# Kernel tuning notes

Hardware: AMD Instinct MI355X
Metric: run time of the kernel (lower is better)

Reference implementation:

```python
import jax, jax.numpy as jnp
import numpy as np

DIM = 512
CODEBOOK_SIZE = 2048
NUM_Q = 8
COMMIT_W = 0.25
B, T = 8, 2048


def setup_inputs() -> dict:
    key = jax.random.key(0)
    k1, k2 = jax.random.split(key)
    x = jax.random.normal(k1, (B, T, DIM), dtype=jnp.float32)
    lim = 1.0 / CODEBOOK_SIZE
    codebooks = jax.random.uniform(k2, (NUM_Q, CODEBOOK_SIZE, DIM), dtype=jnp.float32,
                                   minval=-lim, maxval=lim)
    return {"x": x, "codebooks": codebooks}


def reference(x, codebooks):
    """Residual VQ forward.
    x: (B, T, D); codebooks: (Q, K, D).
    Returns (quantized (B,T,D), indices (B,T,Q) int32, mean loss scalar).
    """
    sg = jax.lax.stop_gradient
    residual = x
    quantized = jnp.zeros_like(x)
    idx_list = []
    total_loss = jnp.zeros((), dtype=x.dtype)
    for i in range(NUM_Q):
        cb = codebooks[i]  # (K, D)
        # squared L2 distances: (B,T,K)
        d = (jnp.sum(residual * residual, axis=-1, keepdims=True)
             - 2.0 * jnp.einsum('btd,kd->btk', residual, cb)
             + jnp.sum(cb * cb, axis=-1))
        min_idx = jnp.argmin(d, axis=-1)  # (B,T)
        idx_list.append(min_idx)
        q_lvl = cb[min_idx]  # (B,T,D) gather
        quantized = quantized + q_lvl
        commit_loss = jnp.mean((sg(residual) - q_lvl) ** 2)
        codebook_loss = jnp.mean((residual - sg(q_lvl)) ** 2)
        total_loss = total_loss + commit_loss * COMMIT_W + codebook_loss
        residual = residual - sg(q_lvl)
    # straight-through estimator
    quantized = x + sg(quantized - x)
    indices = jnp.stack(idx_list, axis=-1)  # (B,T,Q)
    return quantized, indices, total_loss / NUM_Q
```

## Files before the change

kernel.cpp:

```cpp
#include <hip/hip_runtime.h>


constexpr int DIM   = 512;
constexpr int KCB   = 2048;
constexpr int NQ    = 8;
constexpr int NTOK  = 8 * 2048;
constexpr int QELEM = NTOK * DIM;
constexpr int NBLK2 = KCB / 256;
constexpr float WINDOW = 1e-3f;

using short8  = __attribute__((ext_vector_type(8))) short;
using float4v = __attribute__((ext_vector_type(4))) float;

__device__ __forceinline__ unsigned short f2bf(float f) {
    unsigned u = __float_as_uint(f);
    return (unsigned short)((u + 0x7FFFu + ((u >> 16) & 1u)) >> 16);
}

__device__ __forceinline__ void gl2lds16(const void* g, void* l) {
    __builtin_amdgcn_global_load_lds(
        (__attribute__((address_space(1))) void*)g,
        (__attribute__((address_space(3))) void*)l, 16, 0, 0);
}

struct Top4 { float s[4]; int i[4]; };
__device__ __forceinline__ void t4_init(Top4& t) {
#pragma unroll
    for (int j = 0; j < 4; ++j) { t.s[j] = 3.0e38f; t.i[j] = 0x7FFFFFFF; }
}
__device__ __forceinline__ void t4_ins(Top4& t, float s, int idx) {
    if (s < t.s[3]) {
        if (s < t.s[2]) { t.s[3] = t.s[2]; t.i[3] = t.i[2];
            if (s < t.s[1]) { t.s[2] = t.s[1]; t.i[2] = t.i[1];
                if (s < t.s[0]) { t.s[1] = t.s[0]; t.i[1] = t.i[0]; t.s[0] = s; t.i[0] = idx; }
                else            { t.s[1] = s; t.i[1] = idx; }
            } else { t.s[2] = s; t.i[2] = idx; }
        } else { t.s[3] = s; t.i[3] = idx; }
    }
}

__global__ __launch_bounds__(256) void k_initnorm(
        const float* __restrict__ x, const float* __restrict__ cbs,
        float4* __restrict__ R, ushort4* __restrict__ Rb, ushort4* __restrict__ Cbb,
        float* __restrict__ r2, float* __restrict__ c2)
{
#pragma clang fp contract(off)
    __shared__ float buf[4][DIM];
    __shared__ float accs[4][32];
    const int w = threadIdx.x >> 6, lane = threadIdx.x & 63;
    const bool isX = blockIdx.x < (NTOK / 4);
    const int row = (isX ? blockIdx.x : blockIdx.x - NTOK / 4) * 4 + w;

    const float* src = isX ? x : cbs;
    const float4* a4 = reinterpret_cast<const float4*>(src + (size_t)row * DIM);
    float4 v0 = a4[lane], v1 = a4[lane + 64];

    ushort4 b0 = make_ushort4(f2bf(v0.x), f2bf(v0.y), f2bf(v0.z), f2bf(v0.w));
    ushort4 b1 = make_ushort4(f2bf(v1.x), f2bf(v1.y), f2bf(v1.z), f2bf(v1.w));
    if (isX) {
        R [(size_t)row * 128 + lane]      = v0;
        R [(size_t)row * 128 + lane + 64] = v1;
        Rb[(size_t)row * 128 + lane]      = b0;
        Rb[(size_t)row * 128 + lane + 64] = b1;
    } else {
        Cbb[(size_t)row * 128 + lane]      = b0;
        Cbb[(size_t)row * 128 + lane + 64] = b1;
    }

    float4* b4 = reinterpret_cast<float4*>(buf[w]);
    b4[lane]      = v0;
    b4[lane + 64] = v1;
    __syncthreads();
    if (lane < 32) {
        int blk = lane >> 3, j = lane & 7;
        const float* p = buf[w] + blk * 128 + j;
        float x0 = p[0];
        float acc = x0 * x0;
#pragma unroll
        for (int m = 1; m < 16; ++m) { float xx = p[8 * m]; acc = acc + xx * xx; }
        accs[w][lane] = acc;
    }
    __syncthreads();
    if (lane == 0) {
        float B[4];
#pragma unroll
        for (int blk = 0; blk < 4; ++blk) {
            const float* r = &accs[w][blk * 8];
            B[blk] = ((r[0] + r[1]) + (r[2] + r[3])) + ((r[4] + r[5]) + (r[6] + r[7]));
        }
        float out = (B[0] + B[1]) + (B[2] + B[3]);
        if (isX) r2[row] = out; else c2[row] = out;
    }
}

__global__ __launch_bounds__(512, 2) void k_gemm_topk(
        const unsigned short* __restrict__ Rb, const unsigned short* __restrict__ Cbb,
        const float* __restrict__ c2, float* __restrict__ candS, int* __restrict__ candI)
{
    __shared__ __align__(16) char smem[99328];
    unsigned short* As = (unsigned short*)smem;
    unsigned short* Bs = (unsigned short*)(smem + 49152);
    float*  scb = (float*)smem;
    float*  c2s = (float*)(smem + 98304);

    const int tid  = threadIdx.x;
    const int wid  = tid >> 6, lane = tid & 63;
    const int quad = lane >> 4, l16 = lane & 15;
    const int wr = wid >> 2, wc = wid & 3;

    const int L    = blockIdx.y * NBLK2 + blockIdx.x;
    const int slot = L >> 3;
    const int mb   = (L & 7) * 8 + (slot >> 3);
    const int nb2  = slot & 7;

    const int tok0 = mb * 256, n0 = nb2 * 256;

    if (tid < 256) c2s[tid] = c2[n0 + tid];

    float4v acc[8][4];
    float4v zero = {0.f, 0.f, 0.f, 0.f};
#pragma unroll
    for (int mi = 0; mi < 8; ++mi)
#pragma unroll
        for (int nj = 0; nj < 4; ++nj) acc[mi][nj] = zero;

    auto stage = [&](int b3, int kb) {
        unsigned short* Ad = As + b3 * 8192;
        unsigned short* Bd = Bs + b3 * 8192;
#pragma unroll
        for (int c = 0; c < 2; ++c) {
            int g = wid * 2 + c;
            gl2lds16(&Rb[(size_t)(tok0 + g * 16 + l16) * DIM + kb + quad * 8],
                     Ad + (size_t)(g * 64) * 8);
        }
#pragma unroll
        for (int c = 0; c < 2; ++c) {
            int g = wid * 2 + c;
            gl2lds16(&Cbb[(size_t)(n0 + g * 16 + l16) * DIM + kb + quad * 8],
                     Bd + (size_t)(g * 64) * 8);
        }
    };

    auto compute = [&](int b3) {
        const unsigned short* Ac = As + b3 * 8192;
        const unsigned short* Bc = Bs + b3 * 8192;
        short8 af[8], bf[4];
#pragma unroll
        for (int mi = 0; mi < 8; ++mi)
            af[mi] = *(const short8*)(Ac + ((size_t)(wr * 8 + mi) * 64 + lane) * 8);
#pragma unroll
        for (int nj = 0; nj < 4; ++nj)
            bf[nj] = *(const short8*)(Bc + ((size_t)(wc * 4 + nj) * 64 + lane) * 8);
        __builtin_amdgcn_s_setprio(1);
#pragma unroll
        for (int mi = 0; mi < 8; ++mi)
#pragma unroll
            for (int nj = 0; nj < 4; ++nj)
                acc[mi][nj] = __builtin_amdgcn_mfma_f32_16x16x32_bf16(
                    af[mi], bf[nj], acc[mi][nj], 0, 0, 0);
        __builtin_amdgcn_s_setprio(0);
    };

    stage(0, 0);
    stage(1, 32);
    for (int it = 0; it < 16; ++it) {
        if (it < 15) asm volatile("s_waitcnt vmcnt(4)" ::: "memory");
        else         asm volatile("s_waitcnt vmcnt(0)" ::: "memory");
        __builtin_amdgcn_s_barrier();
        __builtin_amdgcn_sched_barrier(0);
        if (it < 14) stage((it + 2) % 3, (it + 2) * 32);
        compute(it % 3);
    }

    const int row_ = tid >> 3, pp = tid & 7;
    float4 c2r[8];
#pragma unroll
    for (int j = 0; j < 8; ++j)
        c2r[j] = *(const float4*)(c2s + pp * 32 + 4 * j);

#pragma unroll
    for (int qr = 0; qr < 4; ++qr) {
        __syncthreads();
        if (wr == (qr >> 1)) {
            const int mi0 = (qr & 1) * 4;
#pragma unroll
            for (int mm = 0; mm < 4; ++mm)
#pragma unroll
                for (int nj = 0; nj < 4; ++nj) {
                    int r0 = mm * 16 + quad * 4;
                    int cc = wc * 64 + nj * 16 + l16;
#pragma unroll
                    for (int e = 0; e < 4; ++e)
                        scb[(r0 + e) * 260 + cc] = acc[mi0 + mm][nj][e];
                }
        }
        __syncthreads();
        Top4 t; t4_init(t);
#pragma unroll
        for (int j = 0; j < 8; ++j) {
            float4 sv = *(const float4*)(scb + row_ * 260 + pp * 32 + 4 * j);
            float4 cv = c2r[j];
            int c0 = n0 + pp * 32 + 4 * j;
            t4_ins(t, cv.x - 2.0f * sv.x, c0 + 0);
            t4_ins(t, cv.y - 2.0f * sv.y, c0 + 1);
            t4_ins(t, cv.z - 2.0f * sv.z, c0 + 2);
            t4_ins(t, cv.w - 2.0f * sv.w, c0 + 3);
        }
#pragma unroll
        for (int k = 1; k <= 2; k <<= 1) {
            float os[4]; int oi[4];
#pragma unroll
            for (int j = 0; j < 4; ++j) {
                os[j] = __shfl_xor(t.s[j], k, 64);
                oi[j] = __shfl_xor(t.i[j], k, 64);
            }
#pragma unroll
            for (int j = 0; j < 4; ++j) t4_ins(t, os[j], oi[j]);
        }
        if ((pp & 3) == 0) {
            int token = tok0 + qr * 64 + row_;
            int nb = nb2 * 2 + (pp >> 2);
            size_t base = (size_t)token * 64 + (size_t)nb * 4;
#pragma unroll
            for (int j = 0; j < 4; ++j) { candS[base + j] = t.s[j]; candI[base + j] = t.i[j]; }
        }
    }
}

__global__ __launch_bounds__(256) void k_selupd(
        const float* __restrict__ candS, const int* __restrict__ candI,
        float* __restrict__ R, const float* __restrict__ cbf,
        float* __restrict__ r2, const float* __restrict__ c2,
        float* __restrict__ idx_out, float* __restrict__ partial,
        ushort4* __restrict__ Rb, const float4* __restrict__ x, int level)
{
#pragma clang fp contract(off)
    __shared__ float buf[4][DIM];
    __shared__ float accs[4][32];
    __shared__ float shl[4];
    const int w = threadIdx.x >> 6, lane = threadIdx.x & 63;
    const int t = blockIdx.x * 4 + w;
    const bool last = (level == NQ - 1);

    float4* r4 = reinterpret_cast<float4*>(R + (size_t)t * DIM);
    float4* b4 = reinterpret_cast<float4*>(buf[w]);
    float4 rr[2];
    rr[0] = r4[lane];      rr[1] = r4[lane + 64];
    b4[lane] = rr[0];      b4[lane + 64] = rr[1];

    float sb = candS[(size_t)t * 64 + lane];
    int   ci = candI[(size_t)t * 64 + lane];
    float mn = sb;
#pragma unroll
    for (int off = 32; off; off >>= 1) mn = fminf(mn, __shfl_xor(mn, off, 64));
    unsigned long long mask = __ballot(sb <= mn + WINDOW);
    int ncand = __popcll(mask);
    int winner;
    if (ncand == 1) {
        winner = __shfl(ci, __ffsll(mask) - 1, 64);
    } else {
        int src = 0;
        if (lane < ncand) {
            unsigned long long mm = mask;
            for (int z = 0; z < lane; ++z) mm &= mm - 1;
            src = __ffsll(mm) - 1;
        }
        int cidx = __shfl(ci, src, 64);
        float s = 3.0e38f;
        int   si = 0x7FFFFFFF;
        if (lane < ncand) {
            const float4* cp4 = reinterpret_cast<const float4*>(cbf + (size_t)cidx * DIM);
            const float4* rp4 = reinterpret_cast<const float4*>(buf[w]);
            float d = 0.f;
#pragma unroll 4
            for (int j = 0; j < DIM / 4; ++j) {
                float4 cv = cp4[j];
                float4 rv = rp4[j];
                d = fmaf(rv.x, cv.x, d);
                d = fmaf(rv.y, cv.y, d);
                d = fmaf(rv.z, cv.z, d);
                d = fmaf(rv.w, cv.w, d);
            }
            float td = 2.0f * d;
            float a  = r2[t] - td;
            s  = a + c2[cidx];
            si = cidx;
        }
#pragma unroll
        for (int off = 32; off; off >>= 1) {
            float ov = __shfl_xor(s, off, 64);
            int   oi = __shfl_xor(si, off, 64);
            if (ov < s || (ov == s && oi < si)) { s = ov; si = oi; }
        }
        winner = si;
    }
    if (lane == 0) idx_out[(size_t)t * NQ + level] = (float)winner;

    const float4* c4 = reinterpret_cast<const float4*>(cbf + (size_t)winner * DIM);
    float ls = 0.f;
#pragma unroll
    for (int i = 0; i < 2; ++i) {
        int d = lane + 64 * i;
        float4 rv = rr[i], cv = c4[d];
        rv.x -= cv.x; rv.y -= cv.y; rv.z -= cv.z; rv.w -= cv.w;
        ls = ls + rv.x * rv.x; ls = ls + rv.y * rv.y;
        ls = ls + rv.z * rv.z; ls = ls + rv.w * rv.w;
        if (!last) {
            r4[d] = rv;
            b4[d] = rv;
            Rb[(size_t)t * 128 + d] = make_ushort4(f2bf(rv.x), f2bf(rv.y),
                                                   f2bf(rv.z), f2bf(rv.w));
        } else {
            float4 xv = x[(size_t)t * 128 + d];
            xv.x -= rv.x; xv.y -= rv.y; xv.z -= rv.z; xv.w -= rv.w;
            r4[d] = xv;
        }
    }

    if (!last) {
        __syncthreads();
        if (lane < 32) {
            int blk = lane >> 3, j = lane & 7;
            const float* p = buf[w] + blk * 128 + j;
            float x0 = p[0];
            float acc = x0 * x0;
#pragma unroll
            for (int m = 1; m < 16; ++m) { float xx = p[8 * m]; acc = acc + xx * xx; }
            accs[w][lane] = acc;
        }
        __syncthreads();
        if (lane == 0) {
            float B[4];
#pragma unroll
            for (int blk = 0; blk < 4; ++blk) {
                const float* r = &accs[w][blk * 8];
                B[blk] = ((r[0] + r[1]) + (r[2] + r[3])) + ((r[4] + r[5]) + (r[6] + r[7]));
            }
            r2[t] = (B[0] + B[1]) + (B[2] + B[3]);
        }
    }

#pragma unroll
    for (int off = 32; off; off >>= 1) ls += __shfl_down(ls, off, 64);
    if (lane == 0) shl[w] = ls;
    __syncthreads();
    if (threadIdx.x == 0) partial[blockIdx.x] = (shl[0] + shl[1]) + (shl[2] + shl[3]);
}

__global__ __launch_bounds__(256) void k_finalize_loss(const float* __restrict__ partial,
                                                       float* __restrict__ loss_out)
{
    double s = 0.0;
    for (int i = threadIdx.x; i < NQ * (NTOK / 4); i += 256) s += (double)partial[i];
#pragma unroll
    for (int off = 32; off; off >>= 1) s += __shfl_down(s, off, 64);
    __shared__ double sh[4];
    if ((threadIdx.x & 63) == 0) sh[threadIdx.x >> 6] = s;
    __syncthreads();
    if (threadIdx.x == 0) {
        double tot = (sh[0] + sh[1]) + (sh[2] + sh[3]);
        loss_out[0] = (float)(tot * 1.25 / ((double)NQ * (double)QELEM));
    }
}

extern "C" void kernel_launch(void* const* d_in, const int* in_sizes, int n_in,
                              void* d_out, int out_size, void* d_ws, size_t ws_size,
                              hipStream_t stream)
{
    const float* x   = (const float*)d_in[0];
    const float* cbs = (const float*)d_in[1];

    float* qout     = (float*)d_out;
    float* idx_out  = qout + QELEM;
    float* loss_out = idx_out + (size_t)NTOK * NQ;
    float* R        = qout;

    char* ws = (char*)d_ws;
    size_t off = 0;
    unsigned short* Rb   = (unsigned short*)(ws + off); off += (size_t)QELEM * 2;
    unsigned short* Cbb  = (unsigned short*)(ws + off); off += (size_t)QELEM * 2;
    float*          c2   = (float*)(ws + off);          off += (size_t)NQ * KCB * 4;
    float*          r2   = (float*)(ws + off);          off += (size_t)NTOK * 4;
    float*          part = (float*)(ws + off);          off += (size_t)NQ * (NTOK / 4) * 4;
    float*          candS= (float*)(ws + off);          off += (size_t)NTOK * 64 * 4;
    int*            candI= (int*)(ws + off);            off += (size_t)NTOK * 64 * 4;

    k_initnorm<<<NTOK / 4 + NQ * KCB / 4, 256, 0, stream>>>(
        x, cbs, (float4*)R, (ushort4*)Rb, (ushort4*)Cbb, r2, c2);

    for (int q = 0; q < NQ; ++q) {
        const float*          cbq  = cbs + (size_t)q * KCB * DIM;
        const unsigned short* cbbq = Cbb + (size_t)q * KCB * DIM;
        const float*          c2q  = c2 + (size_t)q * KCB;
        dim3 g(NBLK2, NTOK / 256);
        k_gemm_topk<<<g, 512, 0, stream>>>(Rb, cbbq, c2q, candS, candI);
        k_selupd<<<NTOK / 4, 256, 0, stream>>>(candS, candI, R, cbq, r2, c2q,
                                               idx_out, part + (size_t)q * (NTOK / 4),
                                               (ushort4*)Rb, (const float4*)x, q);
    }

    k_finalize_loss<<<1, 256, 0, stream>>>(part, loss_out);
}
```

Before: 992.6 us.

## Switch GEMM staging to double-buffered 64-wide K tiles with padded c2 layout

Replaces the triple-buffered K=32 staging pipeline, which used explicit vmcnt waits, with a double-buffered K=64 pipeline that loads two 32-wide halves per stage and synchronises with a plain __syncthreads. The aim is to halve the number of barrier iterations and do more MFMA work per sync. It also pads the shared c2 array by 4 floats per 32 entries to cut LDS bank conflicts on the float4 reads. The cost is LDS growing to about 132 KB per block, which likely allows only one block per CU instead of the two requested by launch_bounds. The plain __syncthreads may also drain outstanding loads and shrink the overlap between loads and compute.

```diff
diff --git a/kernel.cpp b/kernel.cpp
--- a/kernel.cpp
+++ b/kernel.cpp
@@ -97,11 +97,11 @@
         const unsigned short* __restrict__ Rb, const unsigned short* __restrict__ Cbb,
         const float* __restrict__ c2, float* __restrict__ candS, int* __restrict__ candI)
 {
-    __shared__ __align__(16) char smem[99328];
+    __shared__ __align__(16) char smem[132224];
     unsigned short* As = (unsigned short*)smem;
-    unsigned short* Bs = (unsigned short*)(smem + 49152);
+    unsigned short* Bs = (unsigned short*)(smem + 65536);
     float*  scb = (float*)smem;
-    float*  c2s = (float*)(smem + 98304);
+    float*  c2s = (float*)(smem + 131072);
 
     const int tid  = threadIdx.x;
     const int wid  = tid >> 6, lane = tid & 63;
@@ -115,7 +115,7 @@
 
     const int tok0 = mb * 256, n0 = nb2 * 256;
 
-    if (tid < 256) c2s[tid] = c2[n0 + tid];
+    if (tid < 256) c2s[tid + 4 * (tid >> 5)] = c2[n0 + tid];
 
     float4v acc[8][4];
     float4v zero = {0.f, 0.f, 0.f, 0.f};
@@ -124,59 +124,62 @@
 #pragma unroll
         for (int nj = 0; nj < 4; ++nj) acc[mi][nj] = zero;
 
-    auto stage = [&](int b3, int kb) {
-        unsigned short* Ad = As + b3 * 8192;
-        unsigned short* Bd = Bs + b3 * 8192;
+    auto stage = [&](int b, int kb) {
+        unsigned short* Ad = As + b * 16384;
+        unsigned short* Bd = Bs + b * 16384;
 #pragma unroll
         for (int c = 0; c < 2; ++c) {
             int g = wid * 2 + c;
-            gl2lds16(&Rb[(size_t)(tok0 + g * 16 + l16) * DIM + kb + quad * 8],
-                     Ad + (size_t)(g * 64) * 8);
+#pragma unroll
+            for (int h = 0; h < 2; ++h)
+                gl2lds16(&Rb[(size_t)(tok0 + g * 16 + l16) * DIM + kb + h * 32 + quad * 8],
+                         Ad + (size_t)g * 1024 + h * 512);
         }
 #pragma unroll
         for (int c = 0; c < 2; ++c) {
             int g = wid * 2 + c;
-            gl2lds16(&Cbb[(size_t)(n0 + g * 16 + l16) * DIM + kb + quad * 8],
-                     Bd + (size_t)(g * 64) * 8);
+#pragma unroll
+            for (int h = 0; h < 2; ++h)
+                gl2lds16(&Cbb[(size_t)(n0 + g * 16 + l16) * DIM + kb + h * 32 + quad * 8],
+                         Bd + (size_t)g * 1024 + h * 512);
         }
     };
 
-    auto compute = [&](int b3) {
-        const unsigned short* Ac = As + b3 * 8192;
-        const unsigned short* Bc = Bs + b3 * 8192;
-        short8 af[8], bf[4];
-#pragma unroll
-        for (int mi = 0; mi < 8; ++mi)
-            af[mi] = *(const short8*)(Ac + ((size_t)(wr * 8 + mi) * 64 + lane) * 8);
-#pragma unroll
-        for (int nj = 0; nj < 4; ++nj)
-            bf[nj] = *(const short8*)(Bc + ((size_t)(wc * 4 + nj) * 64 + lane) * 8);
-        __builtin_amdgcn_s_setprio(1);
-#pragma unroll
-        for (int mi = 0; mi < 8; ++mi)
+    auto compute = [&](int b) {
+        const unsigned short* Ac = As + b * 16384;
+        const unsigned short* Bc = Bs + b * 16384;
+#pragma unroll
+        for (int kk = 0; kk < 2; ++kk) {
+            short8 af[8], bf[4];
+#pragma unroll
+            for (int mi = 0; mi < 8; ++mi)
+                af[mi] = *(const short8*)(Ac + (size_t)(wr * 8 + mi) * 1024 + kk * 512 + lane * 8);
 #pragma unroll
             for (int nj = 0; nj < 4; ++nj)
-                acc[mi][nj] = __builtin_amdgcn_mfma_f32_16x16x32_bf16(
-                    af[mi], bf[nj], acc[mi][nj], 0, 0, 0);
-        __builtin_amdgcn_s_setprio(0);
+                bf[nj] = *(const short8*)(Bc + (size_t)(wc * 4 + nj) * 1024 + kk * 512 + lane * 8);
+            __builtin_amdgcn_s_setprio(1);
+#pragma unroll
+            for (int mi = 0; mi < 8; ++mi)
+#pragma unroll
+                for (int nj = 0; nj < 4; ++nj)
+                    acc[mi][nj] = __builtin_amdgcn_mfma_f32_16x16x32_bf16(
+                        af[mi], bf[nj], acc[mi][nj], 0, 0, 0);
+            __builtin_amdgcn_s_setprio(0);
+        }
     };
 
     stage(0, 0);
-    stage(1, 32);
-    for (int it = 0; it < 16; ++it) {
-        if (it < 15) asm volatile("s_waitcnt vmcnt(4)" ::: "memory");
-        else         asm volatile("s_waitcnt vmcnt(0)" ::: "memory");
-        __builtin_amdgcn_s_barrier();
-        __builtin_amdgcn_sched_barrier(0);
-        if (it < 14) stage((it + 2) % 3, (it + 2) * 32);
-        compute(it % 3);
+    for (int it = 0; it < 8; ++it) {
+        __syncthreads();
+        if (it < 7) stage((it + 1) & 1, (it + 1) * 64);
+        compute(it & 1);
     }
 
     const int row_ = tid >> 3, pp = tid & 7;
     float4 c2r[8];
 #pragma unroll
     for (int j = 0; j < 8; ++j)
-        c2r[j] = *(const float4*)(c2s + pp * 32 + 4 * j);
+        c2r[j] = *(const float4*)(c2s + pp * 36 + 4 * j);
 
 #pragma unroll
     for (int qr = 0; qr < 4; ++qr) {
```

Measured after the change: 1.027 ms. 3.5% more time.

## Split GEMM main loop into two half-phases interleaving A/B staging with MFMA

Applied to the files above, without the earlier changes.

Restructures the triple-buffered bf16 MFMA main loop so that each iteration runs in two halves: it loads B fragments and half of the A fragments, issues the A-tile prefetch, computes half the MFMAs, then barriers, loads the other A half, issues the B-tile prefetch and computes the rest. The aim is to spread global-to-LDS traffic across the compute phase and cut register pressure from holding eight A fragments at once. It also pads the c2 shared-memory array with four floats every 32 entries to avoid LDS bank conflicts when each thread reads its 32-wide slice. The extra barrier per iteration adds synchronization cost, and the explicit lgkmcnt(0) waits may serialize LDS reads with compute.

```diff
diff --git a/kernel.cpp b/kernel.cpp
--- a/kernel.cpp
+++ b/kernel.cpp
@@ -97,7 +97,7 @@
         const unsigned short* __restrict__ Rb, const unsigned short* __restrict__ Cbb,
         const float* __restrict__ c2, float* __restrict__ candS, int* __restrict__ candI)
 {
-    __shared__ __align__(16) char smem[99328];
+    __shared__ __align__(16) char smem[99456];
     unsigned short* As = (unsigned short*)smem;
     unsigned short* Bs = (unsigned short*)(smem + 49152);
     float*  scb = (float*)smem;
@@ -115,7 +115,7 @@
 
     const int tok0 = mb * 256, n0 = nb2 * 256;
 
-    if (tid < 256) c2s[tid] = c2[n0 + tid];
+    if (tid < 256) c2s[tid + 4 * (tid >> 5)] = c2[n0 + tid];
 
     float4v acc[8][4];
     float4v zero = {0.f, 0.f, 0.f, 0.f};
@@ -124,59 +124,83 @@
 #pragma unroll
         for (int nj = 0; nj < 4; ++nj) acc[mi][nj] = zero;
 
-    auto stage = [&](int b3, int kb) {
-        unsigned short* Ad = As + b3 * 8192;
-        unsigned short* Bd = Bs + b3 * 8192;
+    auto stageA = [&](int b, int kb) {
+        unsigned short* Ad = As + b * 8192;
 #pragma unroll
         for (int c = 0; c < 2; ++c) {
             int g = wid * 2 + c;
             gl2lds16(&Rb[(size_t)(tok0 + g * 16 + l16) * DIM + kb + quad * 8],
-                     Ad + (size_t)(g * 64) * 8);
-        }
+                     Ad + (size_t)g * 512);
+        }
+    };
+    auto stageB = [&](int b, int kb) {
+        unsigned short* Bd = Bs + b * 8192;
 #pragma unroll
         for (int c = 0; c < 2; ++c) {
             int g = wid * 2 + c;
             gl2lds16(&Cbb[(size_t)(n0 + g * 16 + l16) * DIM + kb + quad * 8],
-                     Bd + (size_t)(g * 64) * 8);
+                     Bd + (size_t)g * 512);
         }
     };
 
-    auto compute = [&](int b3) {
-        const unsigned short* Ac = As + b3 * 8192;
-        const unsigned short* Bc = Bs + b3 * 8192;
-        short8 af[8], bf[4];
-#pragma unroll
-        for (int mi = 0; mi < 8; ++mi)
-            af[mi] = *(const short8*)(Ac + ((size_t)(wr * 8 + mi) * 64 + lane) * 8);
-#pragma unroll
-        for (int nj = 0; nj < 4; ++nj)
-            bf[nj] = *(const short8*)(Bc + ((size_t)(wc * 4 + nj) * 64 + lane) * 8);
-        __builtin_amdgcn_s_setprio(1);
-#pragma unroll
-        for (int mi = 0; mi < 8; ++mi)
-#pragma unroll
-            for (int nj = 0; nj < 4; ++nj)
-                acc[mi][nj] = __builtin_amdgcn_mfma_f32_16x16x32_bf16(
-                    af[mi], bf[nj], acc[mi][nj], 0, 0, 0);
-        __builtin_amdgcn_s_setprio(0);
-    };
-
-    stage(0, 0);
-    stage(1, 32);
+    stageA(0, 0);  stageB(0, 0);
+    stageA(1, 32); stageB(1, 32);
+    int cur = 0, pf = 2;
     for (int it = 0; it < 16; ++it) {
         if (it < 15) asm volatile("s_waitcnt vmcnt(4)" ::: "memory");
         else         asm volatile("s_waitcnt vmcnt(0)" ::: "memory");
         __builtin_amdgcn_s_barrier();
         __builtin_amdgcn_sched_barrier(0);
-        if (it < 14) stage((it + 2) % 3, (it + 2) * 32);
-        compute(it % 3);
+
+        const unsigned short* Ac = As + cur * 8192;
+        const unsigned short* Bc = Bs + cur * 8192;
+
+        short8 bf[4], af[4];
+#pragma unroll
+        for (int nj = 0; nj < 4; ++nj)
+            bf[nj] = *(const short8*)(Bc + (size_t)(wc * 4 + nj) * 512 + lane * 8);
+#pragma unroll
+        for (int m = 0; m < 4; ++m)
+            af[m] = *(const short8*)(Ac + (size_t)(wr * 8 + m) * 512 + lane * 8);
+        if (it < 14) stageA(pf, (it + 2) * 32);
+        asm volatile("s_waitcnt lgkmcnt(0)" ::: "memory");
+        __builtin_amdgcn_sched_barrier(0);
+        __builtin_amdgcn_s_setprio(1);
+#pragma unroll
+        for (int m = 0; m < 4; ++m)
+#pragma unroll
+            for (int nj = 0; nj < 4; ++nj)
+                acc[m][nj] = __builtin_amdgcn_mfma_f32_16x16x32_bf16(
+                    af[m], bf[nj], acc[m][nj], 0, 0, 0);
+        __builtin_amdgcn_s_setprio(0);
+        __builtin_amdgcn_s_barrier();
+        __builtin_amdgcn_sched_barrier(0);
+
+        short8 af2[4];
+#pragma unroll
+        for (int m = 0; m < 4; ++m)
+            af2[m] = *(const short8*)(Ac + (size_t)(wr * 8 + 4 + m) * 512 + lane * 8);
+        if (it < 14) stageB(pf, (it + 2) * 32);
+        asm volatile("s_waitcnt lgkmcnt(0)" ::: "memory");
+        __builtin_amdgcn_sched_barrier(0);
+        __builtin_amdgcn_s_setprio(1);
+#pragma unroll
+        for (int m = 0; m < 4; ++m)
+#pragma unroll
+            for (int nj = 0; nj < 4; ++nj)
+                acc[4 + m][nj] = __builtin_amdgcn_mfma_f32_16x16x32_bf16(
+                    af2[m], bf[nj], acc[4 + m][nj], 0, 0, 0);
+        __builtin_amdgcn_s_setprio(0);
+
+        cur = (cur == 2) ? 0 : cur + 1;
+        pf  = (pf  == 2) ? 0 : pf  + 1;
     }
 
     const int row_ = tid >> 3, pp = tid & 7;
     float4 c2r[8];
 #pragma unroll
     for (int j = 0; j < 8; ++j)
-        c2r[j] = *(const float4*)(c2s + pp * 32 + 4 * j);
+        c2r[j] = *(const float4*)(c2s + pp * 36 + 4 * j);
 
 #pragma unroll
     for (int qr = 0; qr < 4; ++qr) {
```

Measured after the change: 988.8 us. No clear change (-0.4%).
